# Kernel optimization log

Hardware: AMD Instinct MI355X
Metric: run time of the kernel (lower is better)

Reference implementation:

```python
import jax, jax.numpy as jnp
import numpy as np

N = 100000      # nodes
E = 1600000     # directed edges (avg degree 16)
F_IN = 128      # in_channels
H = 128         # hidden
G = 64          # graphs in batch


def setup_inputs() -> dict:
    key = jax.random.key(0)
    ks = jax.random.split(key, 9)
    x = jax.random.normal(ks[0], (N, F_IN), dtype=jnp.float32)
    edge_index = jax.random.randint(ks[1], (2, E), 0, N, dtype=jnp.int32)
    batch = jnp.sort(jax.random.randint(ks[2], (N,), 0, G, dtype=jnp.int32))
    # GCNConv weights (glorot-ish scale) and biases
    W1 = jax.random.normal(ks[3], (F_IN, H), dtype=jnp.float32) / np.sqrt(F_IN)
    b1 = jnp.zeros((H,), dtype=jnp.float32)
    W2 = jax.random.normal(ks[4], (H, H // 2), dtype=jnp.float32) / np.sqrt(H)
    b2 = jnp.zeros((H // 2,), dtype=jnp.float32)
    lin_w = jax.random.normal(ks[5], (H // 2, 1), dtype=jnp.float32) / np.sqrt(H // 2)
    lin_b = jnp.zeros((1,), dtype=jnp.float32)
    return {"x": x, "edge_index": edge_index, "batch": batch,
            "W1": W1, "b1": b1, "W2": W2, "b2": b2,
            "lin_w": lin_w, "lin_b": lin_b}


def reference(x, edge_index, batch, W1, b1, W2, b2, lin_w, lin_b):
    n = x.shape[0]
    # GCN default: add self-loops, symmetric deg^-1/2 normalization
    loop = jnp.arange(n, dtype=edge_index.dtype)
    src = jnp.concatenate([edge_index[0], loop])
    dst = jnp.concatenate([edge_index[1], loop])
    deg = jax.ops.segment_sum(jnp.ones_like(dst, dtype=x.dtype), dst, num_segments=n)
    dis = jax.lax.rsqrt(jnp.maximum(deg, 1.0))  # deg >= 1 due to self-loops
    norm = dis[src] * dis[dst]                  # [E+N]

    def gcn_conv(h, W, b):
        h = h @ W                               # transform first (smaller dim on edges)
        m = h[src] * norm[:, None]              # gather + scale  [E+N, d]
        return jax.ops.segment_sum(m, dst, num_segments=n) + b  # scatter-add

    h = jax.nn.relu(gcn_conv(x, W1, b1))        # dropout = identity in eval mode
    h = jax.nn.relu(gcn_conv(h, W2, b2))

    # global_mean_pool over graph ids
    sums = jax.ops.segment_sum(h, batch, num_segments=G)            # [G, H//2]
    cnt = jax.ops.segment_sum(jnp.ones((n,), h.dtype), batch, num_segments=G)
    pooled = sums / jnp.maximum(cnt, 1.0)[:, None]

    return (pooled @ lin_w + lin_b)[:, 0]       # squeeze(-1) -> [G]
```

## Files before the change

### kernel.cpp

```cpp
#include <hip/hip_runtime.h>
#include <hip/hip_fp16.h>


#define DN 512
#define DSHIFT 9
#define SLOT 80

typedef _Float16 half8 __attribute__((ext_vector_type(8)));
typedef _Float16 half4v __attribute__((ext_vector_type(4)));
typedef float f32x4 __attribute__((ext_vector_type(4)));

__device__ __forceinline__ int xcd_swz(int b, int n) {
  int x = b & 7, i = b >> 3;
  int q = n >> 3, r = n & 7;
  return x * q + min(x, r) + i;
}

__global__ __launch_bounds__(1024) void k_split(
    const int* __restrict__ src, const int* __restrict__ dst,
    int* __restrict__ hcnt, int* __restrict__ binned, int E, int NBK, int PB,
    int CAPB, const float* __restrict__ W1, const float* __restrict__ W2,
    _Float16* __restrict__ W1t, _Float16* __restrict__ W2t) {
  __shared__ int h[256];
  int t = threadIdx.x;
  int b = blockIdx.x;
  if (b >= PB) {
    if (b == PB) {
      for (int i = t; i < 128 * 128; i += 1024)
        W1t[(i & 127) * 128 + (i >> 7)] = (_Float16)W1[i];
    } else {
      for (int i = t; i < 128 * 64; i += 1024)
        W2t[(i & 63) * 128 + (i >> 6)] = (_Float16)W2[i];
    }
    return;
  }
  if (t < 256) h[t] = 0;
  __syncthreads();
  int base = b * 8192;
  int pk[8], bk[8];
  bool val[8];
#pragma unroll
  for (int j = 0; j < 8; ++j) {
    int i = base + j * 1024 + t;
    val[j] = (i < E);
    if (val[j]) {
      int s = src[i], d = dst[i];
      bk[j] = d >> DSHIFT;
      pk[j] = (s << DSHIFT) | (d & (DN - 1));
      atomicAdd(&h[bk[j]], 1);
    }
  }
  __syncthreads();
  for (int k = t; k < NBK; k += 1024) hcnt[k * PB + b] = min(h[k], SLOT);
  __syncthreads();
  if (t < 256) h[t] = 0;
  __syncthreads();
#pragma unroll
  for (int j = 0; j < 8; ++j) {
    if (val[j]) {
      int slot = atomicAdd(&h[bk[j]], 1);
      if (slot < SLOT) binned[bk[j] * CAPB + b * SLOT + slot] = pk[j];
    }
  }
}

__global__ __launch_bounds__(1024) void k_bucket(const int* __restrict__ binned,
                                                 const int* __restrict__ hcnt,
                                                 int2* __restrict__ rr,
                                                 float* __restrict__ dis,
                                                 int* __restrict__ esrc,
                                                 int N, int PB, int CAPB) {
  __shared__ int hc[1024];
  __shared__ int lcnt[DN];
  __shared__ int lscan[DN];
  int k = blockIdx.x;
  int t = threadIdx.x;
  int nbase = k << DSHIFT;
  for (int b2 = t; b2 < PB; b2 += 1024) hc[b2] = hcnt[k * PB + b2];
  if (t < DN) lcnt[t] = 0;
  __syncthreads();
  for (int idx = t; idx < CAPB; idx += 1024) {
    int b2 = idx / SLOT, j = idx - b2 * SLOT;
    if (j < hc[b2])
      atomicAdd(&lcnt[binned[k * CAPB + idx] & (DN - 1)], 1);
  }
  __syncthreads();
  if (t < DN) lscan[t] = lcnt[t];
  __syncthreads();
  for (int off = 1; off < DN; off <<= 1) {
    int v = (t < DN && t >= off) ? lscan[t - off] : 0;
    __syncthreads();
    if (t < DN) lscan[t] += v;
    __syncthreads();
  }
  int bstart = k * CAPB;
  if (t < DN) {
    int g = nbase + t;
    if (g < N) {
      int inc = lscan[t];
      int c = lcnt[t];
      rr[g] = make_int2(bstart + inc - c, bstart + inc);
      dis[g] = rsqrtf((float)(c + 1));
    }
    lcnt[t] = lscan[t] - lcnt[t];
  }
  __syncthreads();
  for (int idx = t; idx < CAPB; idx += 1024) {
    int b2 = idx / SLOT, j = idx - b2 * SLOT;
    if (j < hc[b2]) {
      int p = binned[k * CAPB + idx];
      int slot = atomicAdd(&lcnt[p & (DN - 1)], 1);
      esrc[bstart + slot] = (unsigned)p >> DSHIFT;
    }
  }
}

template <int COLS, int K, typename AT, bool SCALE>
__global__ __launch_bounds__(256) void k_gemm(const AT* __restrict__ A,
                                              const _Float16* __restrict__ Wt_g,
                                              const float* __restrict__ dis,
                                              __half* __restrict__ out,
                                              int nrows) {
  constexpr int KP = K + 8;
  __shared__ _Float16 As[64 * KP];
  __shared__ _Float16 Wt[COLS * KP];
  int t = threadIdx.x;
  int row0 = blockIdx.x * 64;

  {
    constexpr int K8 = K / 8;
    for (int i = t; i < COLS * K8; i += 256) {
      int c = i / K8, k8 = (i % K8) * 8;
      *(half8*)&Wt[c * KP + k8] = *(const half8*)&Wt_g[c * K + k8];
    }
  }
  if constexpr (sizeof(AT) == 4) {
    constexpr int F4 = K / 4;
    for (int id = t; id < 64 * F4; id += 256) {
      int r = id / F4, kq = (id % F4) * 4;
      int grow = row0 + r;
      float4 av = (grow < nrows) ? *(const float4*)&A[(size_t)grow * K + kq]
                                 : make_float4(0.f, 0.f, 0.f, 0.f);
      half4v hv = {(_Float16)av.x, (_Float16)av.y, (_Float16)av.z,
                   (_Float16)av.w};
      *(half4v*)&As[r * KP + kq] = hv;
    }
  } else {
    constexpr int H8 = K / 8;
    for (int id = t; id < 64 * H8; id += 256) {
      int r = id / H8, kq = (id % H8) * 8;
      int grow = row0 + r;
      half8 av = (grow < nrows)
                     ? *(const half8*)&A[(size_t)grow * K + kq]
                     : (half8){0, 0, 0, 0, 0, 0, 0, 0};
      *(half8*)&As[r * KP + kq] = av;
    }
  }
  __syncthreads();

  int wave = t >> 6, lane = t & 63;
  int m = lane & 15;
  int quad = lane >> 4;
  constexpr int NT = COLS / 16;

  f32x4 acc[NT];
#pragma unroll
  for (int ct = 0; ct < NT; ++ct) acc[ct] = (f32x4){0.f, 0.f, 0.f, 0.f};

  const _Float16* arow = &As[(wave * 16 + m) * KP + quad * 8];
#pragma unroll
  for (int ks = 0; ks < K; ks += 32) {
    half8 af = *(const half8*)&arow[ks];
#pragma unroll
    for (int ct = 0; ct < NT; ++ct) {
      half8 bf = *(const half8*)&Wt[(ct * 16 + m) * KP + quad * 8 + ks];
      acc[ct] = __builtin_amdgcn_mfma_f32_16x16x32_f16(af, bf, acc[ct], 0, 0, 0);
    }
  }

  __syncthreads();
  _Float16* Ds = As;
  constexpr int DP = COLS + 4;
#pragma unroll
  for (int j = 0; j < 4; ++j) {
    int rl = wave * 16 + quad * 4 + j;
    int gr = row0 + rl;
    float dn = 1.f;
    if constexpr (SCALE) dn = (gr < nrows) ? dis[gr] : 0.f;
#pragma unroll
    for (int ct = 0; ct < NT; ++ct)
      Ds[rl * DP + ct * 16 + m] = (_Float16)(acc[ct][j] * dn);
  }
  __syncthreads();
  constexpr int C8 = COLS / 8;
  for (int id = t; id < 64 * C8; id += 256) {
    int r = id / C8, c8 = (id % C8) * 8;
    int gr = row0 + r;
    if (gr < nrows)
      *(half8*)&out[(size_t)gr * COLS + c8] = *(const half8*)&Ds[r * DP + c8];
  }
}

__global__ __launch_bounds__(256) void k_aggemm(
    const __half* __restrict__ XW, const int2* __restrict__ rr,
    const int* __restrict__ esrc, const float* __restrict__ dis,
    const float* __restrict__ bias, const _Float16* __restrict__ W2t,
    __half* __restrict__ XW2, int N) {
  constexpr int K = 128, KP = K + 8, COLS = 64, NT = COLS / 16;
  __shared__ _Float16 As[64 * KP];
  int t = threadIdx.x;
  int lane = t & 63, wave = t >> 6;
  int bid = xcd_swz((int)blockIdx.x, (int)gridDim.x);
  int row0 = bid * 64;

  int group = lane >> 4;
  int c = (lane & 15) * 8;

  for (int i = 0; i < 16; ++i) {
    int r = wave * 16 + i;
    int node = row0 + r;
    float acc[8];
#pragma unroll
    for (int j = 0; j < 8; ++j) acc[j] = 0.f;
    if (node < N) {
      int2 be = rr[node];
      int end = be.y;
      int e0 = be.x + group;
      int e1 = e0 + 4;
      int s0 = 0, s1 = 0;
      float w0 = 0.f, w1 = 0.f;
      if (e0 < end) { s0 = esrc[e0]; w0 = 1.f; }
      if (e1 < end) { s1 = esrc[e1]; w1 = 1.f; }
      while (e0 < end) {
        float4 r0 = *(const float4*)&XW[(size_t)s0 * 128 + c];
        float4 r1 = *(const float4*)&XW[(size_t)s1 * 128 + c];
        int e2 = e0 + 8, e3 = e1 + 8;
        int s2 = 0, s3 = 0;
        float w2 = 0.f, w3 = 0.f;
        if (e2 < end) { s2 = esrc[e2]; w2 = 1.f; }
        if (e3 < end) { s3 = esrc[e3]; w3 = 1.f; }
        {
          union { float4 f4; __half2 h2[4]; } u;
          u.f4 = r0;
#pragma unroll
          for (int j = 0; j < 4; ++j) {
            float2 f = __half22float2(u.h2[j]);
            acc[2 * j + 0] = fmaf(f.x, w0, acc[2 * j + 0]);
            acc[2 * j + 1] = fmaf(f.y, w0, acc[2 * j + 1]);
          }
          u.f4 = r1;
#pragma unroll
          for (int j = 0; j < 4; ++j) {
            float2 f = __half22float2(u.h2[j]);
            acc[2 * j + 0] = fmaf(f.x, w1, acc[2 * j + 0]);
            acc[2 * j + 1] = fmaf(f.y, w1, acc[2 * j + 1]);
          }
        }
        e0 = e2; s0 = s2; w0 = w2;
        e1 = e3; s1 = s3; w1 = w3;
      }
#pragma unroll
      for (int mm = 16; mm < 64; mm <<= 1) {
#pragma unroll
        for (int j = 0; j < 8; ++j) acc[j] += __shfl_xor(acc[j], mm, 64);
      }
    }
    if (group == 0) {
      half8 hv = (half8){0, 0, 0, 0, 0, 0, 0, 0};
      if (node < N) {
        float dn = dis[node];
        union { float4 f4; __half2 h2[4]; } u;
        u.f4 = *(const float4*)&XW[(size_t)node * 128 + c];
        _Float16* hp = (_Float16*)&hv;
#pragma unroll
        for (int j = 0; j < 4; ++j) {
          float2 f = __half22float2(u.h2[j]);
          hp[2 * j + 0] =
              (_Float16)fmaxf(fmaf(acc[2 * j + 0] + f.x, dn, bias[c + 2 * j + 0]), 0.f);
          hp[2 * j + 1] =
              (_Float16)fmaxf(fmaf(acc[2 * j + 1] + f.y, dn, bias[c + 2 * j + 1]), 0.f);
        }
      }
      *(half8*)&As[r * KP + c] = hv;
    }
  }
  __syncthreads();

  int m = lane & 15, quad = lane >> 4;
  half8 bfr[4][NT];
#pragma unroll
  for (int ks4 = 0; ks4 < 4; ++ks4)
#pragma unroll
    for (int ct = 0; ct < NT; ++ct)
      bfr[ks4][ct] =
          *(const half8*)&W2t[(ct * 16 + m) * K + ks4 * 32 + quad * 8];

  f32x4 acc2[NT];
#pragma unroll
  for (int ct = 0; ct < NT; ++ct) acc2[ct] = (f32x4){0.f, 0.f, 0.f, 0.f};
  const _Float16* arow = &As[(wave * 16 + m) * KP + quad * 8];
#pragma unroll
  for (int ks4 = 0; ks4 < 4; ++ks4) {
    half8 af = *(const half8*)&arow[ks4 * 32];
#pragma unroll
    for (int ct = 0; ct < NT; ++ct)
      acc2[ct] =
          __builtin_amdgcn_mfma_f32_16x16x32_f16(af, bfr[ks4][ct], acc2[ct], 0, 0, 0);
  }
  __syncthreads();
  _Float16* Ds = As;
  constexpr int DP = COLS + 4;
#pragma unroll
  for (int j = 0; j < 4; ++j) {
    int rl = wave * 16 + quad * 4 + j;
    int gr = row0 + rl;
    float dn = (gr < N) ? dis[gr] : 0.f;
#pragma unroll
    for (int ct = 0; ct < NT; ++ct)
      Ds[rl * DP + ct * 16 + m] = (_Float16)(acc2[ct][j] * dn);
  }
  __syncthreads();
  for (int id = t; id < 64 * 8; id += 256) {
    int r = id / 8, c8 = (id % 8) * 8;
    int gr = row0 + r;
    if (gr < N)
      *(half8*)&XW2[(size_t)gr * COLS + c8] = *(const half8*)&Ds[r * DP + c8];
  }
}

template <int COLS, bool FUSE>
__global__ __launch_bounds__(256) void k_agg(const __half* __restrict__ H,
                                             const int2* __restrict__ rr,
                                             const int* __restrict__ esrc,
                                             const float* __restrict__ dis,
                                             const float* __restrict__ bias,
                                             __half* __restrict__ out,
                                             const float* __restrict__ lin_w,
                                             float* __restrict__ dnode, int n) {
  constexpr int LPE = COLS / 8;
  constexpr int NG = 64 / LPE;
  int bid = xcd_swz((int)blockIdx.x, (int)gridDim.x);
  int node = (bid * 256 + (int)threadIdx.x) >> 6;
  if (node >= n) return;
  int lane = threadIdx.x & 63;
  int group = lane / LPE;
  int c = (lane % LPE) * 8;

  float acc[8];
#pragma unroll
  for (int j = 0; j < 8; ++j) acc[j] = 0.f;

  int2 be = rr[node];
  int end = be.y;
  int e0 = be.x + group;
  int e1 = e0 + NG;
  int s0 = 0, s1 = 0;
  float w0 = 0.f, w1 = 0.f;
  if (e0 < end) { s0 = esrc[e0]; w0 = 1.f; }
  if (e1 < end) { s1 = esrc[e1]; w1 = 1.f; }
  while (e0 < end) {
    float4 r0 = *(const float4*)&H[(size_t)s0 * COLS + c];
    float4 r1 = *(const float4*)&H[(size_t)s1 * COLS + c];
    int e2 = e0 + 2 * NG, e3 = e1 + 2 * NG;
    int s2 = 0, s3 = 0;
    float w2 = 0.f, w3 = 0.f;
    if (e2 < end) { s2 = esrc[e2]; w2 = 1.f; }
    if (e3 < end) { s3 = esrc[e3]; w3 = 1.f; }
    {
      union { float4 f4; __half2 h2[4]; } u;
      u.f4 = r0;
#pragma unroll
      for (int j = 0; j < 4; ++j) {
        float2 f = __half22float2(u.h2[j]);
        acc[2 * j + 0] = fmaf(f.x, w0, acc[2 * j + 0]);
        acc[2 * j + 1] = fmaf(f.y, w0, acc[2 * j + 1]);
      }
      u.f4 = r1;
#pragma unroll
      for (int j = 0; j < 4; ++j) {
        float2 f = __half22float2(u.h2[j]);
        acc[2 * j + 0] = fmaf(f.x, w1, acc[2 * j + 0]);
        acc[2 * j + 1] = fmaf(f.y, w1, acc[2 * j + 1]);
      }
    }
    e0 = e2; s0 = s2; w0 = w2;
    e1 = e3; s1 = s3; w1 = w3;
  }
#pragma unroll
  for (int m = LPE; m < 64; m <<= 1) {
#pragma unroll
    for (int j = 0; j < 8; ++j) acc[j] += __shfl_xor(acc[j], m, 64);
  }
  if (group == 0) {
    float dn = dis[node];
    union { float4 f4; __half2 h2[4]; } u;
    u.f4 = *(const float4*)&H[(size_t)node * COLS + c];
    float o[8];
#pragma unroll
    for (int j = 0; j < 4; ++j) {
      float2 f = __half22float2(u.h2[j]);
      o[2 * j + 0] = fmaxf(fmaf(acc[2 * j + 0] + f.x, dn, bias[c + 2 * j + 0]), 0.f);
      o[2 * j + 1] = fmaxf(fmaf(acc[2 * j + 1] + f.y, dn, bias[c + 2 * j + 1]), 0.f);
    }
    if constexpr (FUSE) {
      float part = 0.f;
#pragma unroll
      for (int j = 0; j < 8; ++j) part = fmaf(o[j], lin_w[c + j], part);
      part += __shfl_xor(part, 1, 64);
      part += __shfl_xor(part, 2, 64);
      part += __shfl_xor(part, 4, 64);
      if (lane == 0) dnode[node] = part;
    } else {
      union { __half2 h2[4]; float4 f4; } ov;
#pragma unroll
      for (int j = 0; j < 4; ++j)
        ov.h2[j] = __floats2half2_rn(o[2 * j + 0], o[2 * j + 1]);
      *(float4*)&out[(size_t)node * COLS + c] = ov.f4;
    }
  }
}

__device__ inline int lower_bound_i(const int* a, int n, int v) {
  int lo = 0, hi = n;
  while (lo < hi) {
    int m = (lo + hi) >> 1;
    if (a[m] < v) lo = m + 1; else hi = m;
  }
  return lo;
}

__global__ __launch_bounds__(256) void k_poolfinal(const float* __restrict__ dnode,
                                                   const int* __restrict__ batch,
                                                   const float* __restrict__ lin_b,
                                                   float* __restrict__ out, int N) {
  __shared__ int bounds[2];
  __shared__ float red[4];
  int g = blockIdx.x;
  int t = threadIdx.x;
  if (t == 0) bounds[0] = lower_bound_i(batch, N, g);
  if (t == 1) bounds[1] = lower_bound_i(batch, N, g + 1);
  __syncthreads();
  int lo = bounds[0], hi = bounds[1];
  float s = 0.f;
  for (int i = lo + t; i < hi; i += 256) s += dnode[i];
#pragma unroll
  for (int m = 1; m < 64; m <<= 1) s += __shfl_xor(s, m, 64);
  if ((t & 63) == 0) red[t >> 6] = s;
  __syncthreads();
  if (t == 0) {
    float sum = red[0] + red[1] + red[2] + red[3];
    float cnt = (float)(hi - lo);
    out[g] = sum / fmaxf(cnt, 1.f) + lin_b[0];
  }
}

extern "C" void kernel_launch(void* const* d_in, const int* in_sizes, int n_in,
                              void* d_out, int out_size, void* d_ws, size_t ws_size,
                              hipStream_t stream) {
  const float* x = (const float*)d_in[0];
  const int* edge = (const int*)d_in[1];
  const int* batch = (const int*)d_in[2];
  const float* W1 = (const float*)d_in[3];
  const float* b1 = (const float*)d_in[4];
  const float* W2 = (const float*)d_in[5];
  const float* b2 = (const float*)d_in[6];
  const float* lin_w = (const float*)d_in[7];
  const float* lin_b = (const float*)d_in[8];
  float* out = (float*)d_out;

  const int N = in_sizes[2];
  const int E = in_sizes[1] / 2;
  const int G = out_size;
  const int* esrc_in = edge;
  const int* edst_in = edge + E;

  char* w = (char*)d_ws;
  size_t off = 0;
  auto take = [&](size_t bytes) {
    void* p = w + off;
    off += (bytes + 255) & ~(size_t)255;
    return p;
  };
  const int NBK = (N + DN - 1) / DN;
  const int PB = (E + 8191) / 8192;
  const int CAPB = PB * SLOT;
  int* hcnt = (int*)take((size_t)NBK * PB * 4);
  int2* rr = (int2*)take((size_t)N * 8);
  float* dis = (float*)take((size_t)N * 4);
  int* esrc = (int*)take((size_t)NBK * CAPB * 4);
  __half* XW = (__half*)take((size_t)N * 128 * 2);
  __half* XW2 = (__half*)take((size_t)N * 64 * 2);
  float* dnode = (float*)take((size_t)N * 4);
  _Float16* W1t = (_Float16*)take((size_t)128 * 128 * 2);
  _Float16* W2t = (_Float16*)take((size_t)64 * 128 * 2);
  int* binned = (int*)XW2;
  (void)ws_size;
  (void)n_in;

  int GB = (N + 63) / 64;
  int ab = (int)(((size_t)N * 64 + 255) / 256);

  k_split<<<PB + 2, 1024, 0, stream>>>(esrc_in, edst_in, hcnt, binned, E, NBK,
                                       PB, CAPB, W1, W2, W1t, W2t);
  k_bucket<<<NBK, 1024, 0, stream>>>(binned, hcnt, rr, dis, esrc, N, PB, CAPB);
  k_gemm<128, 128, float, true><<<GB, 256, 0, stream>>>(x, W1t, dis, XW, N);
  k_aggemm<<<GB, 256, 0, stream>>>(XW, rr, esrc, dis, b1, W2t, XW2, N);
  k_agg<64, true><<<ab, 256, 0, stream>>>(XW2, rr, esrc, dis, b2, nullptr,
                                          lin_w, dnode, N);
  k_poolfinal<<<G, 256, 0, stream>>>(dnode, batch, lin_b, out, N);
}
```

Before: 272.0 us.

## Use zero sentinel row for gathers, deepen prefetch, shrink bucket sizes

Adds a zeroed padding row at index N in XW and XW2, so out-of-range edge slots gather that row and plain adds replace the weight-multiplied FMAs. The layer-1 aggregation now keeps four neighbour loads in flight per iteration instead of two, and the self row is loaded early rather than re-read in the epilogue. Bucket parameters are halved (DN 256, SLOT 40, 4096 edges per split block, 512-thread blocks) and the binned scratch now aliases XW. The finalize aggregation is specialised to 64 columns with the fused linear step. Risks include extra register pressure, more split blocks, and possible edge drops if a 40-entry slot overflows, since edges beyond SLOT are discarded.

```diff
diff --git a/kernel.cpp b/kernel.cpp
--- a/kernel.cpp
+++ b/kernel.cpp
@@ -2,9 +2,9 @@
 #include <hip/hip_fp16.h>
 
 
-#define DN 512
-#define DSHIFT 9
-#define SLOT 80
+#define DN 256
+#define DSHIFT 8
+#define SLOT 40
 
 typedef _Float16 half8 __attribute__((ext_vector_type(8)));
 typedef _Float16 half4v __attribute__((ext_vector_type(4)));
@@ -16,32 +16,46 @@
   return x * q + min(x, r) + i;
 }
 
-__global__ __launch_bounds__(1024) void k_split(
+__device__ __forceinline__ void accrow(float* acc, float4 rv) {
+  union { float4 f4; __half2 h2[4]; } u;
+  u.f4 = rv;
+#pragma unroll
+  for (int j = 0; j < 4; ++j) {
+    float2 f = __half22float2(u.h2[j]);
+    acc[2 * j + 0] += f.x;
+    acc[2 * j + 1] += f.y;
+  }
+}
+
+__global__ __launch_bounds__(512) void k_split(
     const int* __restrict__ src, const int* __restrict__ dst,
     int* __restrict__ hcnt, int* __restrict__ binned, int E, int NBK, int PB,
     int CAPB, const float* __restrict__ W1, const float* __restrict__ W2,
-    _Float16* __restrict__ W1t, _Float16* __restrict__ W2t) {
-  __shared__ int h[256];
+    _Float16* __restrict__ W1t, _Float16* __restrict__ W2t,
+    __half* __restrict__ XW, __half* __restrict__ XW2, int N) {
+  __shared__ int h[512];
   int t = threadIdx.x;
   int b = blockIdx.x;
   if (b >= PB) {
     if (b == PB) {
-      for (int i = t; i < 128 * 128; i += 1024)
+      for (int i = t; i < 128 * 128; i += 512)
         W1t[(i & 127) * 128 + (i >> 7)] = (_Float16)W1[i];
     } else {
-      for (int i = t; i < 128 * 64; i += 1024)
+      for (int i = t; i < 128 * 64; i += 512)
         W2t[(i & 63) * 128 + (i >> 6)] = (_Float16)W2[i];
+      if (t < 128) XW[(size_t)N * 128 + t] = __float2half(0.f);
+      if (t < 64) XW2[(size_t)N * 64 + t] = __float2half(0.f);
     }
     return;
   }
-  if (t < 256) h[t] = 0;
-  __syncthreads();
-  int base = b * 8192;
+  h[t] = 0;
+  __syncthreads();
+  int base = b * 4096;
   int pk[8], bk[8];
   bool val[8];
 #pragma unroll
   for (int j = 0; j < 8; ++j) {
-    int i = base + j * 1024 + t;
+    int i = base + j * 512 + t;
     val[j] = (i < E);
     if (val[j]) {
       int s = src[i], d = dst[i];
@@ -51,9 +65,9 @@
     }
   }
   __syncthreads();
-  for (int k = t; k < NBK; k += 1024) hcnt[k * PB + b] = min(h[k], SLOT);
-  __syncthreads();
-  if (t < 256) h[t] = 0;
+  for (int k = t; k < NBK; k += 512) hcnt[k * PB + b] = min(h[k], SLOT);
+  __syncthreads();
+  h[t] = 0;
   __syncthreads();
 #pragma unroll
   for (int j = 0; j < 8; ++j) {
@@ -64,22 +78,22 @@
   }
 }
 
-__global__ __launch_bounds__(1024) void k_bucket(const int* __restrict__ binned,
-                                                 const int* __restrict__ hcnt,
-                                                 int2* __restrict__ rr,
-                                                 float* __restrict__ dis,
-                                                 int* __restrict__ esrc,
-                                                 int N, int PB, int CAPB) {
-  __shared__ int hc[1024];
+__global__ __launch_bounds__(512) void k_bucket(const int* __restrict__ binned,
+                                                const int* __restrict__ hcnt,
+                                                int2* __restrict__ rr,
+                                                float* __restrict__ dis,
+                                                int* __restrict__ esrc,
+                                                int N, int PB, int CAPB) {
+  __shared__ int hc[512];
   __shared__ int lcnt[DN];
   __shared__ int lscan[DN];
   int k = blockIdx.x;
   int t = threadIdx.x;
   int nbase = k << DSHIFT;
-  for (int b2 = t; b2 < PB; b2 += 1024) hc[b2] = hcnt[k * PB + b2];
+  for (int b2 = t; b2 < PB; b2 += 512) hc[b2] = hcnt[k * PB + b2];
   if (t < DN) lcnt[t] = 0;
   __syncthreads();
-  for (int idx = t; idx < CAPB; idx += 1024) {
+  for (int idx = t; idx < CAPB; idx += 512) {
     int b2 = idx / SLOT, j = idx - b2 * SLOT;
     if (j < hc[b2])
       atomicAdd(&lcnt[binned[k * CAPB + idx] & (DN - 1)], 1);
@@ -105,7 +119,7 @@
     lcnt[t] = lscan[t] - lcnt[t];
   }
   __syncthreads();
-  for (int idx = t; idx < CAPB; idx += 1024) {
+  for (int idx = t; idx < CAPB; idx += 512) {
     int b2 = idx / SLOT, j = idx - b2 * SLOT;
     if (j < hc[b2]) {
       int p = binned[k * CAPB + idx];
@@ -222,42 +236,31 @@
     float acc[8];
 #pragma unroll
     for (int j = 0; j < 8; ++j) acc[j] = 0.f;
+    float4 selfv = make_float4(0.f, 0.f, 0.f, 0.f);
     if (node < N) {
       int2 be = rr[node];
       int end = be.y;
-      int e0 = be.x + group;
-      int e1 = e0 + 4;
-      int s0 = 0, s1 = 0;
-      float w0 = 0.f, w1 = 0.f;
-      if (e0 < end) { s0 = esrc[e0]; w0 = 1.f; }
-      if (e1 < end) { s1 = esrc[e1]; w1 = 1.f; }
+      if (group == 0) selfv = *(const float4*)&XW[(size_t)node * 128 + c];
+      int e0 = be.x + group, e1 = e0 + 4, e2 = e0 + 8, e3 = e0 + 12;
+      int s0 = (e0 < end) ? esrc[e0] : N;
+      int s1 = (e1 < end) ? esrc[e1] : N;
+      int s2 = (e2 < end) ? esrc[e2] : N;
+      int s3 = (e3 < end) ? esrc[e3] : N;
       while (e0 < end) {
         float4 r0 = *(const float4*)&XW[(size_t)s0 * 128 + c];
         float4 r1 = *(const float4*)&XW[(size_t)s1 * 128 + c];
-        int e2 = e0 + 8, e3 = e1 + 8;
-        int s2 = 0, s3 = 0;
-        float w2 = 0.f, w3 = 0.f;
-        if (e2 < end) { s2 = esrc[e2]; w2 = 1.f; }
-        if (e3 < end) { s3 = esrc[e3]; w3 = 1.f; }
-        {
-          union { float4 f4; __half2 h2[4]; } u;
-          u.f4 = r0;
-#pragma unroll
-          for (int j = 0; j < 4; ++j) {
-            float2 f = __half22float2(u.h2[j]);
-            acc[2 * j + 0] = fmaf(f.x, w0, acc[2 * j + 0]);
-            acc[2 * j + 1] = fmaf(f.y, w0, acc[2 * j + 1]);
-          }
-          u.f4 = r1;
-#pragma unroll
-          for (int j = 0; j < 4; ++j) {
-            float2 f = __half22float2(u.h2[j]);
-            acc[2 * j + 0] = fmaf(f.x, w1, acc[2 * j + 0]);
-            acc[2 * j + 1] = fmaf(f.y, w1, acc[2 * j + 1]);
-          }
-        }
-        e0 = e2; s0 = s2; w0 = w2;
-        e1 = e3; s1 = s3; w1 = w3;
+        float4 r2 = *(const float4*)&XW[(size_t)s2 * 128 + c];
+        float4 r3 = *(const float4*)&XW[(size_t)s3 * 128 + c];
+        e0 += 16; e1 += 16; e2 += 16; e3 += 16;
+        int n0 = (e0 < end) ? esrc[e0] : N;
+        int n1 = (e1 < end) ? esrc[e1] : N;
+        int n2 = (e2 < end) ? esrc[e2] : N;
+        int n3 = (e3 < end) ? esrc[e3] : N;
+        accrow(acc, r0);
+        accrow(acc, r1);
+        accrow(acc, r2);
+        accrow(acc, r3);
+        s0 = n0; s1 = n1; s2 = n2; s3 = n3;
       }
 #pragma unroll
       for (int mm = 16; mm < 64; mm <<= 1) {
@@ -270,7 +273,7 @@
       if (node < N) {
         float dn = dis[node];
         union { float4 f4; __half2 h2[4]; } u;
-        u.f4 = *(const float4*)&XW[(size_t)node * 128 + c];
+        u.f4 = selfv;
         _Float16* hp = (_Float16*)&hv;
 #pragma unroll
         for (int j = 0; j < 4; ++j) {
@@ -328,23 +331,21 @@
   }
 }
 
-template <int COLS, bool FUSE>
-__global__ __launch_bounds__(256) void k_agg(const __half* __restrict__ H,
-                                             const int2* __restrict__ rr,
-                                             const int* __restrict__ esrc,
-                                             const float* __restrict__ dis,
-                                             const float* __restrict__ bias,
-                                             __half* __restrict__ out,
-                                             const float* __restrict__ lin_w,
-                                             float* __restrict__ dnode, int n) {
-  constexpr int LPE = COLS / 8;
-  constexpr int NG = 64 / LPE;
+__global__ __launch_bounds__(256) void k_aggfin(const __half* __restrict__ H,
+                                                const int2* __restrict__ rr,
+                                                const int* __restrict__ esrc,
+                                                const float* __restrict__ dis,
+                                                const float* __restrict__ bias,
+                                                const float* __restrict__ lin_w,
+                                                float* __restrict__ dnode,
+                                                int n) {
+  constexpr int COLS = 64;
   int bid = xcd_swz((int)blockIdx.x, (int)gridDim.x);
   int node = (bid * 256 + (int)threadIdx.x) >> 6;
   if (node >= n) return;
   int lane = threadIdx.x & 63;
-  int group = lane / LPE;
-  int c = (lane % LPE) * 8;
+  int group = lane >> 3;
+  int c = (lane & 7) * 8;
 
   float acc[8];
 #pragma unroll
@@ -352,71 +353,44 @@
 
   int2 be = rr[node];
   int end = be.y;
+  float4 selfv = make_float4(0.f, 0.f, 0.f, 0.f);
+  if (group == 0) selfv = *(const float4*)&H[(size_t)node * COLS + c];
   int e0 = be.x + group;
-  int e1 = e0 + NG;
-  int s0 = 0, s1 = 0;
-  float w0 = 0.f, w1 = 0.f;
-  if (e0 < end) { s0 = esrc[e0]; w0 = 1.f; }
-  if (e1 < end) { s1 = esrc[e1]; w1 = 1.f; }
+  int e1 = e0 + 8;
+  int s0 = (e0 < end) ? esrc[e0] : n;
+  int s1 = (e1 < end) ? esrc[e1] : n;
   while (e0 < end) {
     float4 r0 = *(const float4*)&H[(size_t)s0 * COLS + c];
     float4 r1 = *(const float4*)&H[(size_t)s1 * COLS + c];
-    int e2 = e0 + 2 * NG, e3 = e1 + 2 * NG;
-    int s2 = 0, s3 = 0;
-    float w2 = 0.f, w3 = 0.f;
-    if (e2 < end) { s2 = esrc[e2]; w2 = 1.f; }
-    if (e3 < end) { s3 = esrc[e3]; w3 = 1.f; }
-    {
-      union { float4 f4; __half2 h2[4]; } u;
-      u.f4 = r0;
-#pragma unroll
-      for (int j = 0; j < 4; ++j) {
-        float2 f = __half22float2(u.h2[j]);
-        acc[2 * j + 0] = fmaf(f.x, w0, acc[2 * j + 0]);
-        acc[2 * j + 1] = fmaf(f.y, w0, acc[2 * j + 1]);
-      }
-      u.f4 = r1;
-#pragma unroll
-      for (int j = 0; j < 4; ++j) {
-        float2 f = __half22float2(u.h2[j]);
-        acc[2 * j + 0] = fmaf(f.x, w1, acc[2 * j + 0]);
-        acc[2 * j + 1] = fmaf(f.y, w1, acc[2 * j + 1]);
-      }
-    }
-    e0 = e2; s0 = s2; w0 = w2;
-    e1 = e3; s1 = s3; w1 = w3;
-  }
-#pragma unroll
-  for (int m = LPE; m < 64; m <<= 1) {
+    e0 += 16; e1 += 16;
+    int t0 = (e0 < end) ? esrc[e0] : n;
+    int t1 = (e1 < end) ? esrc[e1] : n;
+    accrow(acc, r0);
+    accrow(acc, r1);
+    s0 = t0; s1 = t1;
+  }
+#pragma unroll
+  for (int m = 8; m < 64; m <<= 1) {
 #pragma unroll
     for (int j = 0; j < 8; ++j) acc[j] += __shfl_xor(acc[j], m, 64);
   }
   if (group == 0) {
     float dn = dis[node];
     union { float4 f4; __half2 h2[4]; } u;
-    u.f4 = *(const float4*)&H[(size_t)node * COLS + c];
-    float o[8];
+    u.f4 = selfv;
+    float part = 0.f;
 #pragma unroll
     for (int j = 0; j < 4; ++j) {
       float2 f = __half22float2(u.h2[j]);
-      o[2 * j + 0] = fmaxf(fmaf(acc[2 * j + 0] + f.x, dn, bias[c + 2 * j + 0]), 0.f);
-      o[2 * j + 1] = fmaxf(fmaf(acc[2 * j + 1] + f.y, dn, bias[c + 2 * j + 1]), 0.f);
-    }
-    if constexpr (FUSE) {
-      float part = 0.f;
-#pragma unroll
-      for (int j = 0; j < 8; ++j) part = fmaf(o[j], lin_w[c + j], part);
-      part += __shfl_xor(part, 1, 64);
-      part += __shfl_xor(part, 2, 64);
-      part += __shfl_xor(part, 4, 64);
-      if (lane == 0) dnode[node] = part;
-    } else {
-      union { __half2 h2[4]; float4 f4; } ov;
-#pragma unroll
-      for (int j = 0; j < 4; ++j)
-        ov.h2[j] = __floats2half2_rn(o[2 * j + 0], o[2 * j + 1]);
-      *(float4*)&out[(size_t)node * COLS + c] = ov.f4;
-    }
+      float o0 = fmaxf(fmaf(acc[2 * j + 0] + f.x, dn, bias[c + 2 * j + 0]), 0.f);
+      float o1 = fmaxf(fmaf(acc[2 * j + 1] + f.y, dn, bias[c + 2 * j + 1]), 0.f);
+      part = fmaf(o0, lin_w[c + 2 * j + 0], part);
+      part = fmaf(o1, lin_w[c + 2 * j + 1], part);
+    }
+    part += __shfl_xor(part, 1, 64);
+    part += __shfl_xor(part, 2, 64);
+    part += __shfl_xor(part, 4, 64);
+    if (lane == 0) dnode[node] = part;
   }
 }
 
@@ -482,30 +456,29 @@
     return p;
   };
   const int NBK = (N + DN - 1) / DN;
-  const int PB = (E + 8191) / 8192;
+  const int PB = (E + 4095) / 4096;
   const int CAPB = PB * SLOT;
   int* hcnt = (int*)take((size_t)NBK * PB * 4);
   int2* rr = (int2*)take((size_t)N * 8);
   float* dis = (float*)take((size_t)N * 4);
   int* esrc = (int*)take((size_t)NBK * CAPB * 4);
-  __half* XW = (__half*)take((size_t)N * 128 * 2);
-  __half* XW2 = (__half*)take((size_t)N * 64 * 2);
+  __half* XW = (__half*)take((size_t)(N + 1) * 128 * 2);
+  __half* XW2 = (__half*)take((size_t)(N + 1) * 64 * 2);
   float* dnode = (float*)take((size_t)N * 4);
   _Float16* W1t = (_Float16*)take((size_t)128 * 128 * 2);
   _Float16* W2t = (_Float16*)take((size_t)64 * 128 * 2);
-  int* binned = (int*)XW2;
+  int* binned = (int*)XW;
   (void)ws_size;
   (void)n_in;
 
   int GB = (N + 63) / 64;
   int ab = (int)(((size_t)N * 64 + 255) / 256);
 
-  k_split<<<PB + 2, 1024, 0, stream>>>(esrc_in, edst_in, hcnt, binned, E, NBK,
-                                       PB, CAPB, W1, W2, W1t, W2t);
-  k_bucket<<<NBK, 1024, 0, stream>>>(binned, hcnt, rr, dis, esrc, N, PB, CAPB);
+  k_split<<<PB + 2, 512, 0, stream>>>(esrc_in, edst_in, hcnt, binned, E, NBK,
+                                      PB, CAPB, W1, W2, W1t, W2t, XW, XW2, N);
+  k_bucket<<<NBK, 512, 0, stream>>>(binned, hcnt, rr, dis, esrc, N, PB, CAPB);
   k_gemm<128, 128, float, true><<<GB, 256, 0, stream>>>(x, W1t, dis, XW, N);
   k_aggemm<<<GB, 256, 0, stream>>>(XW, rr, esrc, dis, b1, W2t, XW2, N);
-  k_agg<64, true><<<ab, 256, 0, stream>>>(XW2, rr, esrc, dis, b2, nullptr,
-                                          lin_w, dnode, N);
+  k_aggfin<<<ab, 256, 0, stream>>>(XW2, rr, esrc, dis, b2, lin_w, dnode, N);
   k_poolfinal<<<G, 256, 0, stream>>>(dnode, batch, lin_b, out, N);
 }
```

Result: slower. 300.7 us (+10.6%).
